# Optimization experiments

Measured on AMD Instinct MI355X. Metric: run time of the kernel, lower is better.

Reference implementation:

```python
import jax, jax.numpy as jnp
import numpy as np

B, S, IN, D, H, L, M = 8, 1024, 256, 512, 8, 2, 64
DK = D // H
FF = 4 * D
EPS = 1e-5


def setup_inputs() -> dict:
    key = jax.random.key(0)
    ks = jax.random.split(key, 16)
    w = lambda k, shape: jax.random.normal(k, shape, jnp.float32) * 0.02
    return {
        "inputs": jax.random.normal(ks[0], (B, S, IN), jnp.float32),
        "lengths": jax.random.randint(ks[1], (B,), S // 2, S + 1),
        "W_in": w(ks[2], (IN, D)), "b_in": jnp.zeros((D,), jnp.float32),
        # per-layer stacked params (leading axis L) for lax.scan
        "Wq": w(ks[3], (L, D, D)), "bq": jnp.zeros((L, D), jnp.float32),
        "Wk": w(ks[4], (L, D, D)), "bk": jnp.zeros((L, D), jnp.float32),
        "Wv": w(ks[5], (L, D, D)), "bv": jnp.zeros((L, D), jnp.float32),
        "Wo": w(ks[6], (L, D, D)), "bo": jnp.zeros((L, D), jnp.float32),
        "rel_bias": w(ks[7], (L, H, 2 * M - 1)),
        "W1": w(ks[8], (L, D, FF)), "b1": jnp.zeros((L, FF), jnp.float32),
        "W2": w(ks[9], (L, FF, D)), "b2": jnp.zeros((L, D), jnp.float32),
        "g1": jnp.ones((L, D), jnp.float32), "be1": jnp.zeros((L, D), jnp.float32),
        "g2": jnp.ones((L, D), jnp.float32), "be2": jnp.zeros((L, D), jnp.float32),
        "gf": jnp.ones((D,), jnp.float32), "bef": jnp.zeros((D,), jnp.float32),
    }


def _ln(x, g, b):
    m = jnp.mean(x, axis=-1, keepdims=True)
    v = jnp.mean(jnp.square(x - m), axis=-1, keepdims=True)
    return (x - m) * jax.lax.rsqrt(v + EPS) * g + b


def _sinusoid_pe(seq_len, d_model):
    pos = jnp.arange(seq_len, dtype=jnp.float32)[:, None]
    div = jnp.exp(jnp.arange(0, d_model, 2, dtype=jnp.float32) * (-np.log(10000.0) / d_model))
    pe = jnp.zeros((seq_len, d_model), jnp.float32)
    pe = pe.at[:, 0::2].set(jnp.sin(pos * div))
    pe = pe.at[:, 1::2].set(jnp.cos(pos * div))
    return pe


def _encoder(inputs, lengths, W_in, b_in, Wq, bq, Wk, bk, Wv, bv, Wo, bo,
             rel_bias, W1, b1, W2, b2, g1, be1, g2, be2, gf, bef):
    x = inputs @ W_in + b_in                      # (B,S,D)
    x = x + _sinusoid_pe(S, D)[None]
    pad = jnp.arange(S)[None, :] >= lengths[:, None]   # (B,S) True = padded key

    r = jnp.arange(S)
    rel_idx = jnp.clip(r[:, None] - r[None, :], -(M - 1), M - 1) + (M - 1)  # (S,S)
    scale = 1.0 / np.sqrt(DK)

    def layer(x, p):
        (wq, bq_, wk, bk_, wv, bv_, wo, bo_, rb, w1, b1_, w2, b2_, g1_, be1_, g2_, be2_) = p
        # --- self-attention sublayer (pre-norm) ---
        h = _ln(x, g1_, be1_)
        q = (h @ wq + bq_).reshape(B, S, H, DK).transpose(0, 2, 1, 3)  # (B,H,S,DK)
        k = (h @ wk + bk_).reshape(B, S, H, DK).transpose(0, 2, 1, 3)
        v = (h @ wv + bv_).reshape(B, S, H, DK).transpose(0, 2, 1, 3)
        scores = jnp.einsum('bhqd,bhkd->bhqk', q, k) * scale
        scores = scores + rb[:, rel_idx][None]            # (H,S,S) relative bias
        scores = jnp.where(pad[:, None, None, :], -jnp.inf, scores)
        attn = jax.nn.softmax(scores, axis=-1)
        o = jnp.einsum('bhqk,bhkd->bhqd', attn, v)
        o = o.transpose(0, 2, 1, 3).reshape(B, S, D) @ wo + bo_
        x = x + o
        # --- FFN sublayer (pre-norm) ---
        h = _ln(x, g2_, be2_)
        x = x + (jax.nn.relu(h @ w1 + b1_) @ w2 + b2_)
        return x, None

    stacked = (Wq, bq, Wk, bk, Wv, bv, Wo, bo, rel_bias, W1, b1, W2, b2, g1, be1, g2, be2)
    x, _ = jax.lax.scan(layer, x, stacked)
    return _ln(x, gf, bef)


def reference(inputs, lengths, W_in, b_in, Wq, bq, Wk, bk, Wv, bv, Wo, bo,
              rel_bias, W1, b1, W2, b2, g1, be1, g2, be2, gf, bef):
    return _encoder(inputs, lengths, W_in, b_in, Wq, bq, Wk, bk, Wv, bv, Wo, bo,
                    rel_bias, W1, b1, W2, b2, g1, be1, g2, be2, gf, bef)
```

## Files before the change

kernel.cpp:

```cpp
#include <hip/hip_runtime.h>
#include <hip/hip_bf16.h>

typedef unsigned short u16;
typedef __bf16 v8bf __attribute__((ext_vector_type(8)));
typedef float v4f __attribute__((ext_vector_type(4)));

#define B_SZ 8
#define S_LEN 1024
#define IN_DIM 256
#define DMODEL 512
#define NHEAD 8
#define DK 64
#define FF_DIM 2048
#define MROWS (B_SZ * S_LEN)
#define QSCALE 0.1803368801111204f

__device__ __forceinline__ u16 f2bf(float f) {
    unsigned int x = __float_as_uint(f);
    unsigned int r = (x + 0x7fffu + ((x >> 16) & 1u)) >> 16;
    return (u16)r;
}

__device__ __forceinline__ void gl16(const u16* g, u16* l) {
    __builtin_amdgcn_global_load_lds((const __attribute__((address_space(1))) unsigned int*)g,
                                     (__attribute__((address_space(3))) unsigned int*)l, 16, 0, 0);
}

__global__ __launch_bounds__(256) void conv_bf16_kernel(const float* __restrict__ in,
                                                        u16* __restrict__ out, int n4) {
    int i = blockIdx.x * 256 + threadIdx.x;
    if (i < n4) {
        float4 v = ((const float4*)in)[i];
        ushort4 o;
        o.x = f2bf(v.x); o.y = f2bf(v.y); o.z = f2bf(v.z); o.w = f2bf(v.w);
        ((ushort4*)out)[i] = o;
    }
}

struct TDesc { const float* src; u16* dst; int K; int N; };
struct TArgs { TDesc d[13]; };

__global__ void transpose_conv_kernel(TArgs args) {
    TDesc t = args.d[blockIdx.z];
    int k0 = blockIdx.x * 32, n0 = blockIdx.y * 32;
    if (k0 >= t.K || n0 >= t.N) return;
    __shared__ float tile[32][33];
    int tx = threadIdx.x, ty = threadIdx.y;
#pragma unroll
    for (int j = 0; j < 4; j++) {
        int k = k0 + ty + j * 8;
        tile[ty + j * 8][tx] = t.src[(size_t)k * t.N + n0 + tx];
    }
    __syncthreads();
#pragma unroll
    for (int j = 0; j < 4; j++) {
        int n = n0 + ty + j * 8;
        t.dst[(size_t)n * t.K + k0 + tx] = f2bf(tile[tx][ty + j * 8]);
    }
}

template <bool OUT_BF16>
__global__ __launch_bounds__(256) void ln_kernel(const float* __restrict__ x,
                                                 const float* __restrict__ g,
                                                 const float* __restrict__ b,
                                                 void* __restrict__ out) {
    int row = blockIdx.x * 4 + (threadIdx.x >> 6);
    int lane = threadIdx.x & 63;
    const float4* xr = (const float4*)(x + (size_t)row * DMODEL);
    float4 v0 = xr[lane], v1 = xr[lane + 64];
    float s = v0.x + v0.y + v0.z + v0.w + v1.x + v1.y + v1.z + v1.w;
    float sq = v0.x * v0.x + v0.y * v0.y + v0.z * v0.z + v0.w * v0.w +
               v1.x * v1.x + v1.y * v1.y + v1.z * v1.z + v1.w * v1.w;
#pragma unroll
    for (int m = 1; m < 64; m <<= 1) {
        s += __shfl_xor(s, m);
        sq += __shfl_xor(sq, m);
    }
    float mean = s * (1.0f / DMODEL);
    float var = sq * (1.0f / DMODEL) - mean * mean;
    float rstd = rsqrtf(var + 1e-5f);
    const float4* g4 = (const float4*)g;
    const float4* b4 = (const float4*)b;
    float4 ga = g4[lane], gb = g4[lane + 64], ba = b4[lane], bb = b4[lane + 64];
    float4 r0, r1;
    r0.x = (v0.x - mean) * rstd * ga.x + ba.x;
    r0.y = (v0.y - mean) * rstd * ga.y + ba.y;
    r0.z = (v0.z - mean) * rstd * ga.z + ba.z;
    r0.w = (v0.w - mean) * rstd * ga.w + ba.w;
    r1.x = (v1.x - mean) * rstd * gb.x + bb.x;
    r1.y = (v1.y - mean) * rstd * gb.y + bb.y;
    r1.z = (v1.z - mean) * rstd * gb.z + bb.z;
    r1.w = (v1.w - mean) * rstd * gb.w + bb.w;
    if (OUT_BF16) {
        ushort4 o0, o1;
        o0.x = f2bf(r0.x); o0.y = f2bf(r0.y); o0.z = f2bf(r0.z); o0.w = f2bf(r0.w);
        o1.x = f2bf(r1.x); o1.y = f2bf(r1.y); o1.z = f2bf(r1.z); o1.w = f2bf(r1.w);
        ((ushort4*)out)[(size_t)row * 128 + lane] = o0;
        ((ushort4*)out)[(size_t)row * 128 + 64 + lane] = o1;
    } else {
        ((float4*)out)[(size_t)row * 128 + lane] = r0;
        ((float4*)out)[(size_t)row * 128 + 64 + lane] = r1;
    }
}

template <int NT>
__device__ __forceinline__ void gemm_core(const u16* __restrict__ A, const u16* __restrict__ Bt,
                                          int K, v4f (&acc)[4][NT]) {
    constexpr int BN = NT * 32;
    constexpr int NB = NT;
    __shared__ u16 As[128 * 64];
    __shared__ u16 Bs[BN * 64];
    int tid = threadIdx.x;
    int n0 = blockIdx.x * BN, m0 = blockIdx.y * 128;
    int w = tid >> 6, lane = tid & 63;
    int wr = (w >> 1) * 64, wc = (w & 1) * (BN / 2);
    int lr = lane & 15, lq = lane >> 4;
    int r8 = lane >> 3, cb = lane & 7;
    int scol = (cb ^ (r8 & 7)) * 8;

    v4f zero = {0.f, 0.f, 0.f, 0.f};
#pragma unroll
    for (int i = 0; i < 4; i++)
#pragma unroll
        for (int j = 0; j < NT; j++) acc[i][j] = zero;

    const u16* gA[4]; u16* lA[4];
#pragma unroll
    for (int j = 0; j < 4; j++) {
        int row0 = 32 * w + j * 8;
        gA[j] = A + (size_t)(m0 + row0 + r8) * K + scol;
        lA[j] = As + row0 * 64;
    }
    const u16* gB[NB]; u16* lB[NB];
#pragma unroll
    for (int j = 0; j < NB; j++) {
        int row0 = (BN / 4) * w + j * 8;
        gB[j] = Bt + (size_t)(n0 + row0 + r8) * K + scol;
        lB[j] = Bs + row0 * 64;
    }

    for (int k0 = 0; k0 < K; k0 += 64) {
#pragma unroll
        for (int j = 0; j < 4; j++) gl16(gA[j], lA[j]);
#pragma unroll
        for (int j = 0; j < NB; j++) gl16(gB[j], lB[j]);
        __syncthreads();
#pragma unroll
        for (int kk = 0; kk < 2; kk++) {
            int xb = ((kk * 4 + lq) ^ (lr & 7)) * 8;
            v8bf af[4], bfr[NT];
#pragma unroll
            for (int i = 0; i < 4; i++)
                af[i] = *(const v8bf*)&As[(wr + i * 16 + lr) * 64 + xb];
#pragma unroll
            for (int j = 0; j < NT; j++)
                bfr[j] = *(const v8bf*)&Bs[(wc + j * 16 + lr) * 64 + xb];
#pragma unroll
            for (int mt = 0; mt < 4; mt++)
#pragma unroll
                for (int nt = 0; nt < NT; nt++)
                    acc[mt][nt] = __builtin_amdgcn_mfma_f32_16x16x32_bf16(af[mt], bfr[nt], acc[mt][nt], 0, 0, 0);
        }
        __syncthreads();
#pragma unroll
        for (int j = 0; j < 4; j++) gA[j] += 64;
#pragma unroll
        for (int j = 0; j < NB; j++) gB[j] += 64;
    }
}

__global__ __launch_bounds__(256) void gemm_in_kernel(const u16* __restrict__ A,
                                                      const u16* __restrict__ Bt,
                                                      const float* __restrict__ bias,
                                                      float* __restrict__ Out, int K) {
    v4f acc[4][2];
    gemm_core<2>(A, Bt, K, acc);
    int tid = threadIdx.x, w = tid >> 6, lane = tid & 63;
    int lr = lane & 15, lq = lane >> 4;
    int wr = (w >> 1) * 64, wc = (w & 1) * 32;
    int n0 = blockIdx.x * 64, m0 = blockIdx.y * 128;
#pragma unroll
    for (int mt = 0; mt < 4; mt++) {
#pragma unroll
        for (int nt = 0; nt < 2; nt++) {
            int col = n0 + wc + nt * 16 + lr;
            float bcol = bias[col];
            float freq = expf((float)(col & ~1) * (-0.017988946039015984f));
#pragma unroll
            for (int reg = 0; reg < 4; reg++) {
                int row = m0 + wr + mt * 16 + lq * 4 + reg;
                float ang = (float)(row & (S_LEN - 1)) * freq;
                float val = acc[mt][nt][reg] + bcol + ((col & 1) ? cosf(ang) : sinf(ang));
                Out[(size_t)row * DMODEL + col] = val;
            }
        }
    }
}

__global__ __launch_bounds__(256) void gemm_qkv_kernel(const u16* __restrict__ A,
                                                       const u16* __restrict__ Bt,
                                                       const float* __restrict__ bq,
                                                       const float* __restrict__ bk,
                                                       const float* __restrict__ bv,
                                                       u16* __restrict__ Qo,
                                                       u16* __restrict__ Ko,
                                                       u16* __restrict__ Vto, int K) {
    v4f acc[4][4];
    gemm_core<4>(A, Bt, K, acc);
    int tid = threadIdx.x, w = tid >> 6, lane = tid & 63;
    int lr = lane & 15, lq = lane >> 4;
    int wr = (w >> 1) * 64, wc = (w & 1) * 64;
    int n0 = blockIdx.x * 128, m0 = blockIdx.y * 128;
    int seg = n0 >> 9;
#pragma unroll
    for (int mt = 0; mt < 4; mt++) {
#pragma unroll
        for (int nt = 0; nt < 4; nt++) {
            int col = (n0 + wc + nt * 16 + lr) & (DMODEL - 1);
            if (seg == 0) {
                float bcol = bq[col];
#pragma unroll
                for (int reg = 0; reg < 4; reg++) {
                    int row = m0 + wr + mt * 16 + lq * 4 + reg;
                    Qo[(size_t)row * DMODEL + col] = f2bf((acc[mt][nt][reg] + bcol) * QSCALE);
                }
            } else if (seg == 1) {
                float bcol = bk[col];
#pragma unroll
                for (int reg = 0; reg < 4; reg++) {
                    int row = m0 + wr + mt * 16 + lq * 4 + reg;
                    Ko[(size_t)row * DMODEL + col] = f2bf(acc[mt][nt][reg] + bcol);
                }
            } else {
                float bcol = bv[col];
                int row0 = m0 + wr + mt * 16 + lq * 4;
                int bb = row0 >> 10, s0 = row0 & (S_LEN - 1);
                ushort4 o;
                o.x = f2bf(acc[mt][nt][0] + bcol);
                o.y = f2bf(acc[mt][nt][1] + bcol);
                o.z = f2bf(acc[mt][nt][2] + bcol);
                o.w = f2bf(acc[mt][nt][3] + bcol);
                *(ushort4*)(Vto + ((size_t)(bb * DMODEL + col)) * S_LEN + s0) = o;
            }
        }
    }
}

__global__ __launch_bounds__(256) void gemm_relu_kernel(const u16* __restrict__ A,
                                                        const u16* __restrict__ Bt,
                                                        const float* __restrict__ bias,
                                                        u16* __restrict__ Out, int N, int K) {
    v4f acc[4][4];
    gemm_core<4>(A, Bt, K, acc);
    int tid = threadIdx.x, w = tid >> 6, lane = tid & 63;
    int lr = lane & 15, lq = lane >> 4;
    int wr = (w >> 1) * 64, wc = (w & 1) * 64;
    int n0 = blockIdx.x * 128, m0 = blockIdx.y * 128;
#pragma unroll
    for (int mt = 0; mt < 4; mt++) {
#pragma unroll
        for (int nt = 0; nt < 4; nt++) {
            int col = n0 + wc + nt * 16 + lr;
            float bcol = bias[col];
#pragma unroll
            for (int reg = 0; reg < 4; reg++) {
                int row = m0 + wr + mt * 16 + lq * 4 + reg;
                Out[(size_t)row * N + col] = f2bf(fmaxf(acc[mt][nt][reg] + bcol, 0.0f));
            }
        }
    }
}

__global__ __launch_bounds__(256) void gemm_res_kernel(const u16* __restrict__ A,
                                                       const u16* __restrict__ Bt,
                                                       const float* __restrict__ bias,
                                                       float* __restrict__ Out, int K) {
    v4f acc[4][2];
    gemm_core<2>(A, Bt, K, acc);
    int tid = threadIdx.x, w = tid >> 6, lane = tid & 63;
    int lr = lane & 15, lq = lane >> 4;
    int wr = (w >> 1) * 64, wc = (w & 1) * 32;
    int n0 = blockIdx.x * 64, m0 = blockIdx.y * 128;
#pragma unroll
    for (int mt = 0; mt < 4; mt++) {
#pragma unroll
        for (int nt = 0; nt < 2; nt++) {
            int col = n0 + wc + nt * 16 + lr;
            float bcol = bias[col];
#pragma unroll
            for (int reg = 0; reg < 4; reg++) {
                int row = m0 + wr + mt * 16 + lq * 4 + reg;
                size_t idx = (size_t)row * DMODEL + col;
                Out[idx] = Out[idx] + acc[mt][nt][reg] + bcol;
            }
        }
    }
}

#define LDT 72
#define LDP 68
__global__ __launch_bounds__(256) void fattn_kernel(const u16* __restrict__ Qg,
                                                    const u16* __restrict__ Kg,
                                                    const u16* __restrict__ Vtg,
                                                    const float* __restrict__ rb,
                                                    const int* __restrict__ lengths,
                                                    u16* __restrict__ O) {
    int qt = blockIdx.x, h = blockIdx.y, b = blockIdx.z;
    int tid = threadIdx.x, w = tid >> 6, lane = tid & 63;
    int lr = lane & 15, lq = lane >> 4;
    __shared__ u16 Ks[64 * LDT];
    __shared__ u16 Vs[64 * LDT];
    __shared__ u16 Pw[4][32 * LDP];
    __shared__ float rbs[128];
    int len = lengths[b];
    if (tid < 127) rbs[tid] = rb[h * 127 + tid] * 1.4426950408889634f;

    int qw = qt * 128 + w * 32;
    v8bf qa[2][2];
#pragma unroll
    for (int ntq = 0; ntq < 2; ntq++) {
        size_t qrow = ((size_t)(b * S_LEN + qw + ntq * 16 + lr)) * DMODEL + h * DK;
        qa[ntq][0] = *(const v8bf*)(Qg + qrow + lq * 8);
        qa[ntq][1] = *(const v8bf*)(Qg + qrow + 32 + lq * 8);
    }

    v4f zero = {0.f, 0.f, 0.f, 0.f};
    v4f Oacc[2][4];
#pragma unroll
    for (int mt = 0; mt < 2; mt++)
#pragma unroll
        for (int nt = 0; nt < 4; nt++) Oacc[mt][nt] = zero;
    float lsum[2] = {0.f, 0.f};

    const u16* Kbase = Kg + ((size_t)b * S_LEN) * DMODEL + h * DK;
    const u16* Vbase = Vtg + ((size_t)(b * DMODEL + h * DK)) * S_LEN;
    u16* P = Pw[w];
    int sr = tid >> 3, sc = (tid & 7) * 8;

    for (int kb0 = 0; kb0 < len; kb0 += 64) {
        __syncthreads();
#pragma unroll
        for (int j = 0; j < 2; j++) {
            int rr = sr + j * 32;
            *(v8bf*)&Ks[rr * LDT + sc] = *(const v8bf*)(Kbase + (size_t)(kb0 + rr) * DMODEL + sc);
            *(v8bf*)&Vs[rr * LDT + sc] = *(const v8bf*)(Vbase + (size_t)rr * S_LEN + kb0 + sc);
        }
        __syncthreads();

        v8bf kf[4][2];
#pragma unroll
        for (int mtk = 0; mtk < 4; mtk++) {
            kf[mtk][0] = *(const v8bf*)&Ks[(mtk * 16 + lr) * LDT + lq * 8];
            kf[mtk][1] = *(const v8bf*)&Ks[(mtk * 16 + lr) * LDT + 32 + lq * 8];
        }

        v4f S[4][2];
#pragma unroll
        for (int mtk = 0; mtk < 4; mtk++)
#pragma unroll
            for (int ntq = 0; ntq < 2; ntq++) {
                v4f s = __builtin_amdgcn_mfma_f32_16x16x32_bf16(kf[mtk][0], qa[ntq][0], zero, 0, 0, 0);
                S[mtk][ntq] = __builtin_amdgcn_mfma_f32_16x16x32_bf16(kf[mtk][1], qa[ntq][1], s, 0, 0, 0);
            }

        bool edge = (kb0 + 64 > len);
        int dmin = qw - (kb0 + 63), dmax = qw + 31 - kb0;
        bool perel = !(dmax <= -63 || dmin >= 63);
        float bconst = (dmax <= -63) ? rbs[0] : rbs[126];
#pragma unroll
        for (int mtk = 0; mtk < 4; mtk++) {
#pragma unroll
            for (int ntq = 0; ntq < 2; ntq++) {
                int q = qw + ntq * 16 + lr;
                ushort4 pk;
#pragma unroll
                for (int r = 0; r < 4; r++) {
                    int key = kb0 + mtk * 16 + lq * 4 + r;
                    float s = S[mtk][ntq][r];
                    if (perel) {
                        int d = q - key;
                        d = d < -63 ? -63 : (d > 63 ? 63 : d);
                        s += rbs[d + 63];
                    } else {
                        s += bconst;
                    }
                    float p = exp2f(s);
                    if (edge && key >= len) p = 0.f;
                    lsum[ntq] += p;
                    ((u16*)&pk)[r] = f2bf(p);
                }
                *(ushort4*)&P[(ntq * 16 + lr) * LDP + mtk * 16 + lq * 4] = pk;
            }
        }

        v8bf vb[4][2];
#pragma unroll
        for (int ntd = 0; ntd < 4; ntd++) {
            vb[ntd][0] = *(const v8bf*)&Vs[(ntd * 16 + lr) * LDT + lq * 8];
            vb[ntd][1] = *(const v8bf*)&Vs[(ntd * 16 + lr) * LDT + 32 + lq * 8];
        }
#pragma unroll
        for (int mtq = 0; mtq < 2; mtq++) {
            v8bf pa0 = *(const v8bf*)&P[(mtq * 16 + lr) * LDP + lq * 8];
            v8bf pa1 = *(const v8bf*)&P[(mtq * 16 + lr) * LDP + 32 + lq * 8];
#pragma unroll
            for (int ntd = 0; ntd < 4; ntd++) {
                Oacc[mtq][ntd] = __builtin_amdgcn_mfma_f32_16x16x32_bf16(pa0, vb[ntd][0], Oacc[mtq][ntd], 0, 0, 0);
                Oacc[mtq][ntd] = __builtin_amdgcn_mfma_f32_16x16x32_bf16(pa1, vb[ntd][1], Oacc[mtq][ntd], 0, 0, 0);
            }
        }
    }

    float lsumR[2];
#pragma unroll
    for (int ntq = 0; ntq < 2; ntq++) {
        float s = lsum[ntq];
        s += __shfl_xor(s, 16);
        s += __shfl_xor(s, 32);
        lsumR[ntq] = s;
    }
#pragma unroll
    for (int mtq = 0; mtq < 2; mtq++) {
        float inv[4];
#pragma unroll
        for (int r = 0; r < 4; r++)
            inv[r] = 1.0f / __shfl(lsumR[mtq], lq * 4 + r);
        size_t obase = ((size_t)(b * S_LEN + qw + mtq * 16)) * DMODEL + h * DK;
#pragma unroll
        for (int ntd = 0; ntd < 4; ntd++)
#pragma unroll
            for (int r = 0; r < 4; r++)
                O[obase + (size_t)(lq * 4 + r) * DMODEL + ntd * 16 + lr] = f2bf(Oacc[mtq][ntd][r] * inv[r]);
    }
}

extern "C" void kernel_launch(void* const* d_in, const int* in_sizes, int n_in,
                              void* d_out, int out_size, void* d_ws, size_t ws_size,
                              hipStream_t stream) {
    const float* inputs   = (const float*)d_in[0];
    const int*   lengths  = (const int*)d_in[1];
    const float* W_in     = (const float*)d_in[2];
    const float* b_in     = (const float*)d_in[3];
    const float* Wq       = (const float*)d_in[4];
    const float* bq       = (const float*)d_in[5];
    const float* Wk       = (const float*)d_in[6];
    const float* bk       = (const float*)d_in[7];
    const float* Wv       = (const float*)d_in[8];
    const float* bv       = (const float*)d_in[9];
    const float* Wo       = (const float*)d_in[10];
    const float* bo       = (const float*)d_in[11];
    const float* rel_bias = (const float*)d_in[12];
    const float* W1       = (const float*)d_in[13];
    const float* b1       = (const float*)d_in[14];
    const float* W2       = (const float*)d_in[15];
    const float* b2       = (const float*)d_in[16];
    const float* g1       = (const float*)d_in[17];
    const float* be1      = (const float*)d_in[18];
    const float* g2       = (const float*)d_in[19];
    const float* be2      = (const float*)d_in[20];
    const float* gf       = (const float*)d_in[21];
    const float* bef      = (const float*)d_in[22];

    char* ws = (char*)d_ws;
    float* xbuf = (float*)ws;          ws += (size_t)MROWS * DMODEL * 4;
    u16* hbuf   = (u16*)ws;            ws += (size_t)MROWS * DMODEL * 2;
    u16* aobuf  = (u16*)ws;            ws += (size_t)MROWS * DMODEL * 2;
    u16* qbf    = (u16*)ws;
    u16* kbf    = qbf + (size_t)MROWS * DMODEL;
    u16* vtbf   = kbf + (size_t)MROWS * DMODEL;
    u16* tbuf   = qbf;                 ws += (size_t)MROWS * DMODEL * 4 * 3;
    u16* inbf   = (u16*)ws;            ws += (size_t)MROWS * IN_DIM * 2;
    u16* wt_in  = (u16*)ws;            ws += (size_t)DMODEL * IN_DIM * 2;
    u16 *qkvw[2], *wto[2], *wt1[2], *wt2[2];
    for (int l = 0; l < 2; l++) { qkvw[l] = (u16*)ws; ws += (size_t)3 * DMODEL * DMODEL * 2; }
    for (int l = 0; l < 2; l++) { wto[l] = (u16*)ws; ws += (size_t)DMODEL * DMODEL * 2; }
    for (int l = 0; l < 2; l++) { wt1[l] = (u16*)ws; ws += (size_t)FF_DIM * DMODEL * 2; }
    for (int l = 0; l < 2; l++) { wt2[l] = (u16*)ws; ws += (size_t)DMODEL * FF_DIM * 2; }

    TArgs ta;
    int ti = 0;
    ta.d[ti++] = {W_in, wt_in, IN_DIM, DMODEL};
    for (int l = 0; l < 2; l++) {
        ta.d[ti++] = {Wq + (size_t)l * DMODEL * DMODEL, qkvw[l], DMODEL, DMODEL};
        ta.d[ti++] = {Wk + (size_t)l * DMODEL * DMODEL, qkvw[l] + (size_t)DMODEL * DMODEL, DMODEL, DMODEL};
        ta.d[ti++] = {Wv + (size_t)l * DMODEL * DMODEL, qkvw[l] + (size_t)2 * DMODEL * DMODEL, DMODEL, DMODEL};
        ta.d[ti++] = {Wo + (size_t)l * DMODEL * DMODEL, wto[l], DMODEL, DMODEL};
        ta.d[ti++] = {W1 + (size_t)l * DMODEL * FF_DIM, wt1[l], DMODEL, FF_DIM};
        ta.d[ti++] = {W2 + (size_t)l * FF_DIM * DMODEL, wt2[l], FF_DIM, DMODEL};
    }

    conv_bf16_kernel<<<dim3((MROWS * IN_DIM / 4 + 255) / 256), 256, 0, stream>>>(
        inputs, inbf, MROWS * IN_DIM / 4);
    transpose_conv_kernel<<<dim3(64, 64, 13), dim3(32, 8), 0, stream>>>(ta);

    gemm_in_kernel<<<dim3(DMODEL / 64, MROWS / 128), 256, 0, stream>>>(
        inbf, wt_in, b_in, xbuf, IN_DIM);

    for (int l = 0; l < 2; l++) {
        ln_kernel<true><<<MROWS / 4, 256, 0, stream>>>(xbuf, g1 + l * DMODEL, be1 + l * DMODEL, hbuf);
        gemm_qkv_kernel<<<dim3(3 * DMODEL / 128, MROWS / 128), 256, 0, stream>>>(
            hbuf, qkvw[l], bq + l * DMODEL, bk + l * DMODEL, bv + l * DMODEL,
            qbf, kbf, vtbf, DMODEL);
        fattn_kernel<<<dim3(S_LEN / 128, NHEAD, B_SZ), 256, 0, stream>>>(
            qbf, kbf, vtbf, rel_bias + (size_t)l * NHEAD * 127, lengths, aobuf);
        gemm_res_kernel<<<dim3(DMODEL / 64, MROWS / 128), 256, 0, stream>>>(
            aobuf, wto[l], bo + l * DMODEL, xbuf, DMODEL);
        ln_kernel<true><<<MROWS / 4, 256, 0, stream>>>(xbuf, g2 + l * DMODEL, be2 + l * DMODEL, hbuf);
        gemm_relu_kernel<<<dim3(FF_DIM / 128, MROWS / 128), 256, 0, stream>>>(
            hbuf, wt1[l], b1 + l * FF_DIM, tbuf, FF_DIM, DMODEL);
        gemm_res_kernel<<<dim3(DMODEL / 64, MROWS / 128), 256, 0, stream>>>(
            tbuf, wt2[l], b2 + l * DMODEL, xbuf, FF_DIM);
    }
    ln_kernel<false><<<MROWS / 4, 256, 0, stream>>>(xbuf, gf, bef, d_out);
}
```

Baseline: 491.0 us.

## Use async LDS loads with swizzle in attention, bigger FFN1 tile, fast PE intrinsics

Attention now stages K and V tiles through direct global-to-LDS loads into an XOR-swizzled unpadded layout, replacing register-staged copies into padded shared memory. The probability values are packed to bf16 by truncation rather than round-to-nearest, and exp2 uses the hardware intrinsic. The GEMM core is generalized over its M tile, and the FFN up-projection moves to 256-row tiles. The input projection computes positional encoding with the hardware sin, cos and exp2 intrinsics. The goal is less staging overhead in attention and more operand reuse in the largest GEMM, at the cost of truncation error in P, lower-accuracy trig, and higher register pressure.

```diff
diff --git a/kernel.cpp b/kernel.cpp
--- a/kernel.cpp
+++ b/kernel.cpp
@@ -2,6 +2,7 @@
 #include <hip/hip_bf16.h>
 
 typedef unsigned short u16;
+typedef unsigned int u32;
 typedef __bf16 v8bf __attribute__((ext_vector_type(8)));
 typedef float v4f __attribute__((ext_vector_type(4)));
 
@@ -103,69 +104,69 @@
     }
 }
 
-template <int NT>
+template <int MT, int NT>
 __device__ __forceinline__ void gemm_core(const u16* __restrict__ A, const u16* __restrict__ Bt,
-                                          int K, v4f (&acc)[4][NT]) {
+                                          int K, v4f (&acc)[MT][NT]) {
+    constexpr int BM = MT * 32;
     constexpr int BN = NT * 32;
-    constexpr int NB = NT;
-    __shared__ u16 As[128 * 64];
+    __shared__ u16 As[BM * 64];
     __shared__ u16 Bs[BN * 64];
     int tid = threadIdx.x;
-    int n0 = blockIdx.x * BN, m0 = blockIdx.y * 128;
+    int n0 = blockIdx.x * BN, m0 = blockIdx.y * BM;
     int w = tid >> 6, lane = tid & 63;
-    int wr = (w >> 1) * 64, wc = (w & 1) * (BN / 2);
+    int wr = (w >> 1) * (BM / 2), wc = (w & 1) * (BN / 2);
     int lr = lane & 15, lq = lane >> 4;
     int r8 = lane >> 3, cb = lane & 7;
-    int scol = (cb ^ (r8 & 7)) * 8;
+    int scol = (cb ^ r8) * 8;
 
     v4f zero = {0.f, 0.f, 0.f, 0.f};
 #pragma unroll
-    for (int i = 0; i < 4; i++)
+    for (int i = 0; i < MT; i++)
 #pragma unroll
         for (int j = 0; j < NT; j++) acc[i][j] = zero;
 
-    const u16* gA[4]; u16* lA[4];
-#pragma unroll
-    for (int j = 0; j < 4; j++) {
-        int row0 = 32 * w + j * 8;
+    const u16* gA[MT]; u16* lA[MT];
+#pragma unroll
+    for (int j = 0; j < MT; j++) {
+        int row0 = (MT * 8) * w + j * 8;
         gA[j] = A + (size_t)(m0 + row0 + r8) * K + scol;
         lA[j] = As + row0 * 64;
     }
-    const u16* gB[NB]; u16* lB[NB];
-#pragma unroll
-    for (int j = 0; j < NB; j++) {
-        int row0 = (BN / 4) * w + j * 8;
+    const u16* gB[NT]; u16* lB[NT];
+#pragma unroll
+    for (int j = 0; j < NT; j++) {
+        int row0 = (NT * 8) * w + j * 8;
         gB[j] = Bt + (size_t)(n0 + row0 + r8) * K + scol;
         lB[j] = Bs + row0 * 64;
     }
 
     for (int k0 = 0; k0 < K; k0 += 64) {
 #pragma unroll
-        for (int j = 0; j < 4; j++) gl16(gA[j], lA[j]);
-#pragma unroll
-        for (int j = 0; j < NB; j++) gl16(gB[j], lB[j]);
+        for (int j = 0; j < MT; j++) gl16(gA[j], lA[j]);
+#pragma unroll
+        for (int j = 0; j < NT; j++) gl16(gB[j], lB[j]);
         __syncthreads();
 #pragma unroll
         for (int kk = 0; kk < 2; kk++) {
             int xb = ((kk * 4 + lq) ^ (lr & 7)) * 8;
-            v8bf af[4], bfr[NT];
-#pragma unroll
-            for (int i = 0; i < 4; i++)
+            v8bf af[MT], bfr[NT];
+#pragma unroll
+            for (int i = 0; i < MT; i++)
                 af[i] = *(const v8bf*)&As[(wr + i * 16 + lr) * 64 + xb];
 #pragma unroll
             for (int j = 0; j < NT; j++)
                 bfr[j] = *(const v8bf*)&Bs[(wc + j * 16 + lr) * 64 + xb];
 #pragma unroll
-            for (int mt = 0; mt < 4; mt++)
+            for (int mt = 0; mt < MT; mt++)
 #pragma unroll
                 for (int nt = 0; nt < NT; nt++)
                     acc[mt][nt] = __builtin_amdgcn_mfma_f32_16x16x32_bf16(af[mt], bfr[nt], acc[mt][nt], 0, 0, 0);
         }
         __syncthreads();
 #pragma unroll
-        for (int j = 0; j < 4; j++) gA[j] += 64;
-#pragma unroll
-        for (int j = 0; j < NB; j++) gB[j] += 64;
+        for (int j = 0; j < MT; j++) gA[j] += 64;
+#pragma unroll
+        for (int j = 0; j < NT; j++) gB[j] += 64;
     }
 }
 
@@ -174,7 +175,7 @@
                                                       const float* __restrict__ bias,
                                                       float* __restrict__ Out, int K) {
     v4f acc[4][2];
-    gemm_core<2>(A, Bt, K, acc);
+    gemm_core<4, 2>(A, Bt, K, acc);
     int tid = threadIdx.x, w = tid >> 6, lane = tid & 63;
     int lr = lane & 15, lq = lane >> 4;
     int wr = (w >> 1) * 64, wc = (w & 1) * 32;
@@ -185,13 +186,14 @@
         for (int nt = 0; nt < 2; nt++) {
             int col = n0 + wc + nt * 16 + lr;
             float bcol = bias[col];
-            float freq = expf((float)(col & ~1) * (-0.017988946039015984f));
+            float freq = __builtin_amdgcn_exp2f((float)(col & ~1) * (-0.025953277f));
 #pragma unroll
             for (int reg = 0; reg < 4; reg++) {
                 int row = m0 + wr + mt * 16 + lq * 4 + reg;
-                float ang = (float)(row & (S_LEN - 1)) * freq;
-                float val = acc[mt][nt][reg] + bcol + ((col & 1) ? cosf(ang) : sinf(ang));
-                Out[(size_t)row * DMODEL + col] = val;
+                float rev = (float)(row & (S_LEN - 1)) * freq * 0.15915494309189535f;
+                float fr = __builtin_amdgcn_fractf(rev);
+                float pe = (col & 1) ? __builtin_amdgcn_cosf(fr) : __builtin_amdgcn_sinf(fr);
+                Out[(size_t)row * DMODEL + col] = acc[mt][nt][reg] + bcol + pe;
             }
         }
     }
@@ -206,7 +208,7 @@
                                                        u16* __restrict__ Ko,
                                                        u16* __restrict__ Vto, int K) {
     v4f acc[4][4];
-    gemm_core<4>(A, Bt, K, acc);
+    gemm_core<4, 4>(A, Bt, K, acc);
     int tid = threadIdx.x, w = tid >> 6, lane = tid & 63;
     int lr = lane & 15, lq = lane >> 4;
     int wr = (w >> 1) * 64, wc = (w & 1) * 64;
@@ -250,14 +252,14 @@
                                                         const u16* __restrict__ Bt,
                                                         const float* __restrict__ bias,
                                                         u16* __restrict__ Out, int N, int K) {
-    v4f acc[4][4];
-    gemm_core<4>(A, Bt, K, acc);
+    v4f acc[8][4];
+    gemm_core<8, 4>(A, Bt, K, acc);
     int tid = threadIdx.x, w = tid >> 6, lane = tid & 63;
     int lr = lane & 15, lq = lane >> 4;
-    int wr = (w >> 1) * 64, wc = (w & 1) * 64;
-    int n0 = blockIdx.x * 128, m0 = blockIdx.y * 128;
-#pragma unroll
-    for (int mt = 0; mt < 4; mt++) {
+    int wr = (w >> 1) * 128, wc = (w & 1) * 64;
+    int n0 = blockIdx.x * 128, m0 = blockIdx.y * 256;
+#pragma unroll
+    for (int mt = 0; mt < 8; mt++) {
 #pragma unroll
         for (int nt = 0; nt < 4; nt++) {
             int col = n0 + wc + nt * 16 + lr;
@@ -276,7 +278,7 @@
                                                        const float* __restrict__ bias,
                                                        float* __restrict__ Out, int K) {
     v4f acc[4][2];
-    gemm_core<2>(A, Bt, K, acc);
+    gemm_core<4, 2>(A, Bt, K, acc);
     int tid = threadIdx.x, w = tid >> 6, lane = tid & 63;
     int lr = lane & 15, lq = lane >> 4;
     int wr = (w >> 1) * 64, wc = (w & 1) * 32;
@@ -297,7 +299,6 @@
     }
 }
 
-#define LDT 72
 #define LDP 68
 __global__ __launch_bounds__(256) void fattn_kernel(const u16* __restrict__ Qg,
                                                     const u16* __restrict__ Kg,
@@ -308,8 +309,8 @@
     int qt = blockIdx.x, h = blockIdx.y, b = blockIdx.z;
     int tid = threadIdx.x, w = tid >> 6, lane = tid & 63;
     int lr = lane & 15, lq = lane >> 4;
-    __shared__ u16 Ks[64 * LDT];
-    __shared__ u16 Vs[64 * LDT];
+    __shared__ u16 Ks[64 * 64];
+    __shared__ u16 Vs[64 * 64];
     __shared__ u16 Pw[4][32 * LDP];
     __shared__ float rbs[128];
     int len = lengths[b];
@@ -335,23 +336,27 @@
     const u16* Kbase = Kg + ((size_t)b * S_LEN) * DMODEL + h * DK;
     const u16* Vbase = Vtg + ((size_t)(b * DMODEL + h * DK)) * S_LEN;
     u16* P = Pw[w];
-    int sr = tid >> 3, sc = (tid & 7) * 8;
+    int r8 = lane >> 3, cb = lane & 7;
+    int swz = (cb ^ r8) * 8;
 
     for (int kb0 = 0; kb0 < len; kb0 += 64) {
         __syncthreads();
 #pragma unroll
         for (int j = 0; j < 2; j++) {
-            int rr = sr + j * 32;
-            *(v8bf*)&Ks[rr * LDT + sc] = *(const v8bf*)(Kbase + (size_t)(kb0 + rr) * DMODEL + sc);
-            *(v8bf*)&Vs[rr * LDT + sc] = *(const v8bf*)(Vbase + (size_t)rr * S_LEN + kb0 + sc);
+            int row0 = w * 16 + j * 8;
+            gl16(Kbase + (size_t)(kb0 + row0 + r8) * DMODEL + swz, Ks + row0 * 64);
+            gl16(Vbase + (size_t)(row0 + r8) * S_LEN + kb0 + swz, Vs + row0 * 64);
         }
         __syncthreads();
 
         v8bf kf[4][2];
 #pragma unroll
         for (int mtk = 0; mtk < 4; mtk++) {
-            kf[mtk][0] = *(const v8bf*)&Ks[(mtk * 16 + lr) * LDT + lq * 8];
-            kf[mtk][1] = *(const v8bf*)&Ks[(mtk * 16 + lr) * LDT + 32 + lq * 8];
+#pragma unroll
+            for (int half = 0; half < 2; half++) {
+                int xb = ((half * 4 + lq) ^ (lr & 7)) * 8;
+                kf[mtk][half] = *(const v8bf*)&Ks[(mtk * 16 + lr) * 64 + xb];
+            }
         }
 
         v4f S[4][2];
@@ -372,7 +377,7 @@
 #pragma unroll
             for (int ntq = 0; ntq < 2; ntq++) {
                 int q = qw + ntq * 16 + lr;
-                ushort4 pk;
+                float p[4];
 #pragma unroll
                 for (int r = 0; r < 4; r++) {
                     int key = kb0 + mtk * 16 + lq * 4 + r;
@@ -384,20 +389,26 @@
                     } else {
                         s += bconst;
                     }
-                    float p = exp2f(s);
-                    if (edge && key >= len) p = 0.f;
-                    lsum[ntq] += p;
-                    ((u16*)&pk)[r] = f2bf(p);
+                    float pv = __builtin_amdgcn_exp2f(s);
+                    if (edge && key >= len) pv = 0.f;
+                    lsum[ntq] += pv;
+                    p[r] = pv;
                 }
-                *(ushort4*)&P[(ntq * 16 + lr) * LDP + mtk * 16 + lq * 4] = pk;
+                uint2 pk;
+                pk.x = (__float_as_uint(p[1]) & 0xffff0000u) | (__float_as_uint(p[0]) >> 16);
+                pk.y = (__float_as_uint(p[3]) & 0xffff0000u) | (__float_as_uint(p[2]) >> 16);
+                *(uint2*)&P[(ntq * 16 + lr) * LDP + mtk * 16 + lq * 4] = pk;
             }
         }
 
         v8bf vb[4][2];
 #pragma unroll
         for (int ntd = 0; ntd < 4; ntd++) {
-            vb[ntd][0] = *(const v8bf*)&Vs[(ntd * 16 + lr) * LDT + lq * 8];
-            vb[ntd][1] = *(const v8bf*)&Vs[(ntd * 16 + lr) * LDT + 32 + lq * 8];
+#pragma unroll
+            for (int half = 0; half < 2; half++) {
+                int xb = ((half * 4 + lq) ^ (lr & 7)) * 8;
+                vb[ntd][half] = *(const v8bf*)&Vs[(ntd * 16 + lr) * 64 + xb];
+            }
         }
 #pragma unroll
         for (int mtq = 0; mtq < 2; mtq++) {
@@ -506,7 +517,7 @@
         gemm_res_kernel<<<dim3(DMODEL / 64, MROWS / 128), 256, 0, stream>>>(
             aobuf, wto[l], bo + l * DMODEL, xbuf, DMODEL);
         ln_kernel<true><<<MROWS / 4, 256, 0, stream>>>(xbuf, g2 + l * DMODEL, be2 + l * DMODEL, hbuf);
-        gemm_relu_kernel<<<dim3(FF_DIM / 128, MROWS / 128), 256, 0, stream>>>(
+        gemm_relu_kernel<<<dim3(FF_DIM / 128, MROWS / 256), 256, 0, stream>>>(
             hbuf, wt1[l], b1 + l * FF_DIM, tbuf, FF_DIM, DMODEL);
         gemm_res_kernel<<<dim3(DMODEL / 64, MROWS / 128), 256, 0, stream>>>(
             tbuf, wt2[l], b2 + l * DMODEL, xbuf, FF_DIM);
```

Result: no change. 500.0 us (+1.8%).
